# Kernel optimization log

Hardware: AMD Instinct MI355X
Metric: run time of the kernel (lower is better)

Reference implementation:

```python
import jax, jax.numpy as jnp
import numpy as np

B, S, D_MODEL = 2, 2048, 1024
N_HEADS, D_HEAD = 16, 64
ATTN_SCALE = float(np.sqrt(D_HEAD))
IGNORE = -100000.0


def setup_inputs() -> dict:
    key = jax.random.key(0)
    ks = jax.random.split(key, 8)
    scale = 1.0 / np.sqrt(D_MODEL)
    return {
        "x": jax.random.normal(ks[0], (B, S, D_MODEL), jnp.float32),
        "pos_embed": jax.random.normal(ks[1], (B, S, D_MODEL), jnp.float32),
        "W_Q": jax.random.normal(ks[2], (N_HEADS, D_MODEL, D_HEAD), jnp.float32) * scale,
        "b_Q": jnp.zeros((N_HEADS, D_HEAD), jnp.float32),
        "W_K": jax.random.normal(ks[3], (N_HEADS, D_MODEL, D_HEAD), jnp.float32) * scale,
        "b_K": jnp.zeros((N_HEADS, D_HEAD), jnp.float32),
        "W_V": jax.random.normal(ks[4], (N_HEADS, D_MODEL, D_HEAD), jnp.float32) * scale,
        "b_V": jnp.zeros((N_HEADS, D_HEAD), jnp.float32),
        "W_O": jax.random.normal(ks[5], (N_HEADS, D_HEAD, D_MODEL), jnp.float32) * (1.0 / np.sqrt(D_HEAD)),
        "b_O": jnp.zeros((D_MODEL,), jnp.float32),
    }


def reference(x, pos_embed, W_Q, b_Q, W_K, b_K, W_V, b_V, W_O, b_O):
    # use_pos_resid=False: q,k read x+pos_embed, v reads x
    attn_input = x + pos_embed                                   # [b,p,m]
    q = jnp.einsum('bpm,imh->bpih', attn_input, W_Q) + b_Q       # [b,p,i,h]
    k = jnp.einsum('bpm,imh->bpih', attn_input, W_K) + b_K
    v = jnp.einsum('bpm,imh->bpih', x, W_V) + b_V
    # scores[b,i,p,q]: query index p attends to key index q
    scores = jnp.einsum('bpih,bqih->bipq', q, k) / ATTN_SCALE
    S_len = scores.shape[-1]
    causal = jnp.tril(jnp.ones((S_len, S_len), bool))
    scores = jnp.where(causal, scores, IGNORE)
    attn = jax.nn.softmax(scores, axis=-1)                       # [b,i,q_dst,p_src]
    z = jnp.einsum('bpih,biqp->bqih', v, attn)                   # [b,q,i,h]
    out = jnp.einsum('bqih,ihm->bqm', z, W_O) + b_O              # [b,q,m]
    return out
```

## Files before the change

kernel.cpp:

```cpp
#include <hip/hip_runtime.h>
#include <hip/hip_bf16.h>
#include <stdint.h>

typedef __hip_bfloat16 bf16;
typedef __attribute__((ext_vector_type(8))) short short8;
typedef __attribute__((ext_vector_type(4))) short short4v;
typedef __attribute__((ext_vector_type(4))) float f32x4;
typedef __attribute__((ext_vector_type(16))) float f32x16;
typedef __attribute__((ext_vector_type(4))) unsigned uint4v;
typedef __attribute__((ext_vector_type(2))) unsigned uint2v;

#define AS1 __attribute__((address_space(1)))
#define AS3 __attribute__((address_space(3)))

static constexpr int SEQ = 2048, DM = 1024, DHD = 64;
static constexpr int MROWS = 2 * SEQ;

__device__ __forceinline__ short f2b(float f) {
  __hip_bfloat16 h = __float2bfloat16(f);
  return *reinterpret_cast<short*>(&h);
}

__device__ __forceinline__ unsigned pack2(float lo, float hi) {
  float2 fv; fv.x = lo; fv.y = hi;
  union { __hip_bfloat162 h; unsigned u; } cv;
  cv.h = __float22bfloat162_rn(fv);
  return cv.u;
}

__device__ __forceinline__ float fexp2(float x) {
#if __has_builtin(__builtin_amdgcn_exp2f)
  return __builtin_amdgcn_exp2f(x);
#else
  return exp2f(x);
#endif
}

union U8 { uint4v u; short8 s; };

#define GL16(dst, ptr, off) \
  asm volatile("global_load_dwordx4 %0, %1, off offset:" #off : "=v"(dst) : "v"(ptr))
#define WAITV(n) do { asm volatile("s_waitcnt vmcnt(" #n ")"); __builtin_amdgcn_sched_barrier(0); } while (0)

__device__ __forceinline__ float xmax32(float v) {
#if __has_builtin(__builtin_amdgcn_permlane32_swap)
  uint2v r = __builtin_amdgcn_permlane32_swap(__float_as_uint(v), __float_as_uint(v), false, false);
  return fmaxf(__uint_as_float(r[0]), __uint_as_float(r[1]));
#else
  return fmaxf(v, __shfl_xor(v, 32));
#endif
}
__device__ __forceinline__ float xsum32(float v) {
#if __has_builtin(__builtin_amdgcn_permlane32_swap)
  uint2v r = __builtin_amdgcn_permlane32_swap(__float_as_uint(v), __float_as_uint(v), false, false);
  return __uint_as_float(r[0]) + __uint_as_float(r[1]);
#else
  return v + __shfl_xor(v, 32);
#endif
}

__global__ __launch_bounds__(256) void prep_inputs(const float* __restrict__ x,
                                                   const float* __restrict__ pos,
                                                   bf16* __restrict__ xb,
                                                   bf16* __restrict__ aib) {
  int i = blockIdx.x * 256 + threadIdx.x;
  const int n4 = MROWS * DM / 4;
  if (i >= n4) return;
  f32x4 xv = ((const f32x4*)x)[i];
  f32x4 pv = ((const f32x4*)pos)[i];
  short4v xo, ao;
#pragma unroll
  for (int j = 0; j < 4; ++j) {
    xo[j] = f2b(xv[j]);
    ao[j] = f2b(xv[j] + pv[j]);
  }
  ((short4v*)xb)[i] = xo;
  ((short4v*)aib)[i] = ao;
}

__global__ __launch_bounds__(256) void transpose_w(const float* __restrict__ in,
                                                   bf16* __restrict__ out, int R, int C) {
  __shared__ float t[64][65];
  int ct = blockIdx.x, rt = blockIdx.y, z = blockIdx.z;
  in += (size_t)z * R * C;
  out += (size_t)z * R * C;
  int c = threadIdx.x & 63, g = threadIdx.x >> 6;
#pragma unroll
  for (int j = 0; j < 16; ++j) {
    int r = g * 16 + j;
    t[r][c] = in[(size_t)(rt * 64 + r) * C + (ct * 64 + c)];
  }
  __syncthreads();
#pragma unroll
  for (int j = 0; j < 16; ++j) {
    int rr = g * 16 + j;
    out[(size_t)(ct * 64 + rr) * R + (rt * 64 + c)] = __float2bfloat16(t[c][rr]);
  }
}

template <int MODE, typename OutT>
__device__ __forceinline__ void gemm128_body(const bf16* __restrict__ A,
                                             const bf16* __restrict__ Bt,
                                             const float* __restrict__ bias,
                                             OutT* __restrict__ C, int mt, int nt,
                                             float scale) {
  __shared__ alignas(16) bf16 Al[128 * 32];
  __shared__ alignas(16) bf16 Bl[128 * 32];
  const int lane = threadIdx.x & 63, wv = threadIdx.x >> 6;
  const int wr = wv >> 1, wc = wv & 1;
  const bf16* Ab = A + (size_t)mt * 128 * DM;
  const bf16* Bb = Bt + (size_t)nt * 128 * DM;

  f32x4 acc[4][4];
#pragma unroll
  for (int i = 0; i < 4; ++i)
#pragma unroll
    for (int j = 0; j < 4; ++j) acc[i][j] = (f32x4){0.f, 0.f, 0.f, 0.f};

  for (int kt = 0; kt < DM / 32; ++kt) {
    int k0 = kt * 32;
#pragma unroll
    for (int c = 0; c < 2; ++c) {
      int li0 = wv * 64 + c * 256;
      int li = li0 + lane;
      int row = li >> 2, sl = li & 3;
      int gs = sl ^ ((row >> 1) & 3);
      __builtin_amdgcn_global_load_lds((const AS1 void*)(Ab + (size_t)row * DM + k0 + gs * 8),
                                       (AS3 void*)(&Al[li0 * 8]), 16, 0, 0);
    }
#pragma unroll
    for (int c = 0; c < 2; ++c) {
      int li0 = wv * 64 + c * 256;
      int li = li0 + lane;
      int row = li >> 2, sl = li & 3;
      int gs = sl ^ ((row >> 1) & 3);
      __builtin_amdgcn_global_load_lds((const AS1 void*)(Bb + (size_t)row * DM + k0 + gs * 8),
                                       (AS3 void*)(&Bl[li0 * 8]), 16, 0, 0);
    }
    __syncthreads();

    short8 af[4], bfr[4];
    const int kb = lane >> 4;
#pragma unroll
    for (int mi = 0; mi < 4; ++mi) {
      int r = wr * 64 + mi * 16 + (lane & 15);
      af[mi] = *(const short8*)(&Al[r * 32 + ((kb ^ ((r >> 1) & 3)) << 3)]);
    }
#pragma unroll
    for (int ni = 0; ni < 4; ++ni) {
      int r = wc * 64 + ni * 16 + (lane & 15);
      bfr[ni] = *(const short8*)(&Bl[r * 32 + ((kb ^ ((r >> 1) & 3)) << 3)]);
    }
#pragma unroll
    for (int mi = 0; mi < 4; ++mi)
#pragma unroll
      for (int ni = 0; ni < 4; ++ni)
        acc[mi][ni] = __builtin_amdgcn_mfma_f32_16x16x32_bf16(af[mi], bfr[ni], acc[mi][ni], 0, 0, 0);
    __syncthreads();
  }

#pragma unroll
  for (int mi = 0; mi < 4; ++mi) {
#pragma unroll
    for (int ni = 0; ni < 4; ++ni) {
      int row0 = mt * 128 + wr * 64 + mi * 16 + (lane >> 4) * 4;
      int col = nt * 128 + wc * 64 + ni * 16 + (lane & 15);
      float bv = bias[col];
      if constexpr (MODE == 1) {
#pragma unroll
        for (int j = 0; j < 4; ++j)
          C[(size_t)(row0 + j) * DM + col] = (acc[mi][ni][j] + bv) * scale;
      } else {
        int bb = row0 >> 11, s0 = row0 & 2047;
        int hh = col >> 6, d0 = col & 63;
        size_t bhb = (size_t)(bb * 16 + hh) * 131072;
        if constexpr (MODE == 3) {
          int kc = d0 >> 4, hi = (d0 >> 3) & 1, e = d0 & 7;
          int g = s0 >> 5, r0 = s0 & 31;
          size_t bbase = bhb + g * 2048 + kc * 512 + e;
#pragma unroll
          for (int j = 0; j < 4; ++j)
            ((bf16*)C)[bbase + (size_t)(r0 + j + 32 * hi) * 8] =
                __float2bfloat16((acc[mi][ni][j] + bv) * scale);
        } else {
          int dj = d0 >> 5, d32 = d0 & 31;
          int ks = s0 >> 4, hi2 = (s0 >> 3) & 1, e0 = s0 & 7;
          short4v o;
#pragma unroll
          for (int j = 0; j < 4; ++j) o[j] = f2b(acc[mi][ni][j] + bv);
          *(short4v*)((bf16*)C + bhb + dj * 65536 + ks * 512 + (size_t)(d32 + 32 * hi2) * 8 + e0) = o;
        }
      }
    }
  }
}

static constexpr float QSCALE = 0.125f * 1.4426950408889634f;

__global__ __launch_bounds__(256) void qkv_gemm(const bf16* __restrict__ aib,
                                                const bf16* __restrict__ xb,
                                                const bf16* __restrict__ wqt,
                                                const bf16* __restrict__ wkt,
                                                const bf16* __restrict__ wvt,
                                                const float* __restrict__ bq,
                                                const float* __restrict__ bk,
                                                const float* __restrict__ bv,
                                                bf16* __restrict__ FQ, bf16* __restrict__ FK,
                                                bf16* __restrict__ FV) {
  int mt = blockIdx.x & 31;
  int nt = (blockIdx.x >> 5) & 7;
  int mat = blockIdx.x >> 8;
  if (mat == 0) {
    gemm128_body<3>(aib, wqt, bq, FQ, mt, nt, QSCALE);
  } else if (mat == 1) {
    gemm128_body<3>(aib, wkt, bk, FK, mt, nt, 1.0f);
  } else {
    gemm128_body<4>(xb, wvt, bv, FV, mt, nt, 1.0f);
  }
}

__global__ __launch_bounds__(256) void o_gemm64(const bf16* __restrict__ A,
                                                const bf16* __restrict__ Bt,
                                                const float* __restrict__ bias,
                                                float* __restrict__ out) {
  __shared__ alignas(16) bf16 Al[64 * 32];
  __shared__ alignas(16) bf16 Bl[128 * 32];
  const int mt = blockIdx.x & 63, nt = blockIdx.x >> 6;
  const int lane = threadIdx.x & 63, wv = threadIdx.x >> 6;
  const int wr = wv >> 1, wc = wv & 1;
  const bf16* Ab = A + (size_t)mt * 64 * DM;
  const bf16* Bb = Bt + (size_t)nt * 128 * DM;

  f32x4 acc[2][4];
#pragma unroll
  for (int i = 0; i < 2; ++i)
#pragma unroll
    for (int j = 0; j < 4; ++j) acc[i][j] = (f32x4){0.f, 0.f, 0.f, 0.f};

  for (int kt = 0; kt < DM / 32; ++kt) {
    int k0 = kt * 32;
    {
      int li0 = wv * 64;
      int li = li0 + lane;
      int row = li >> 2, sl = li & 3;
      int gs = sl ^ ((row >> 1) & 3);
      __builtin_amdgcn_global_load_lds((const AS1 void*)(Ab + (size_t)row * DM + k0 + gs * 8),
                                       (AS3 void*)(&Al[li0 * 8]), 16, 0, 0);
    }
#pragma unroll
    for (int c = 0; c < 2; ++c) {
      int li0 = wv * 64 + c * 256;
      int li = li0 + lane;
      int row = li >> 2, sl = li & 3;
      int gs = sl ^ ((row >> 1) & 3);
      __builtin_amdgcn_global_load_lds((const AS1 void*)(Bb + (size_t)row * DM + k0 + gs * 8),
                                       (AS3 void*)(&Bl[li0 * 8]), 16, 0, 0);
    }
    __syncthreads();

    short8 af[2], bfr[4];
    const int kb = lane >> 4;
#pragma unroll
    for (int mi = 0; mi < 2; ++mi) {
      int r = wr * 32 + mi * 16 + (lane & 15);
      af[mi] = *(const short8*)(&Al[r * 32 + ((kb ^ ((r >> 1) & 3)) << 3)]);
    }
#pragma unroll
    for (int ni = 0; ni < 4; ++ni) {
      int r = wc * 64 + ni * 16 + (lane & 15);
      bfr[ni] = *(const short8*)(&Bl[r * 32 + ((kb ^ ((r >> 1) & 3)) << 3)]);
    }
#pragma unroll
    for (int mi = 0; mi < 2; ++mi)
#pragma unroll
      for (int ni = 0; ni < 4; ++ni)
        acc[mi][ni] = __builtin_amdgcn_mfma_f32_16x16x32_bf16(af[mi], bfr[ni], acc[mi][ni], 0, 0, 0);
    __syncthreads();
  }

#pragma unroll
  for (int mi = 0; mi < 2; ++mi) {
#pragma unroll
    for (int ni = 0; ni < 4; ++ni) {
      int row0 = mt * 64 + wr * 32 + mi * 16 + (lane >> 4) * 4;
      int col = nt * 128 + wc * 64 + ni * 16 + (lane & 15);
      float bv = bias[col];
#pragma unroll
      for (int j = 0; j < 4; ++j)
        out[(size_t)(row0 + j) * DM + col] = acc[mi][ni][j] + bv;
    }
  }
}

__global__ __launch_bounds__(128, 2) void flash_attn(const bf16* __restrict__ FQ,
                                                     const bf16* __restrict__ FK,
                                                     const bf16* __restrict__ FV,
                                                     bf16* __restrict__ Zb) {
  __shared__ float Zm[64][33];
  __shared__ float Ml[64], Ll[64];
  __shared__ unsigned Zl[32 * 32];

  const int lane = threadIdx.x & 63;
  const int wvi = threadIdx.x >> 6;
  const int qln = lane & 31;
  const bool hib = lane >= 32;
  const int bh = blockIdx.x & 31;
  const int wq = 63 - (blockIdx.x >> 5);
  const int bb = bh >> 4, h = bh & 15;
  const int q0 = wq * 32;
  const int nt = wq / 2 + 1;
  const int hsp = (nt + 1) >> 1;
  const int t0 = wvi ? hsp : 0;
  const int t1 = wvi ? nt : hsp;

  const size_t fb = (size_t)bh * 131072;
  const bf16* qp = FQ + fb + wq * 2048 + lane * 8;
  const bf16* kpt = FK + fb + (size_t)t0 * 4096 + lane * 8;
  const bf16* vp0 = FV + fb + (size_t)t0 * 2048 + lane * 8;
  const bf16* vp1 = vp0 + 65536;

  f32x16 zacc[2];
#pragma unroll
  for (int i = 0; i < 16; ++i) { zacc[0][i] = 0.f; zacc[1][i] = 0.f; }
  float mrun = -1e30f, lrun = 0.f;

  short8 qf[4];
  short8 kfA[2][4], kfB[2][4];

  if (t0 < t1) {
    GL16(qf[0], qp, 0); GL16(qf[1], qp, 1024); GL16(qf[2], qp, 2048); GL16(qf[3], qp, 3072);
    {
      const bf16* k1 = kpt + 2048;
      GL16(kfA[0][0], kpt, 0); GL16(kfA[0][1], kpt, 1024); GL16(kfA[0][2], kpt, 2048); GL16(kfA[0][3], kpt, 3072);
      GL16(kfA[1][0], k1, 0);  GL16(kfA[1][1], k1, 1024);  GL16(kfA[1][2], k1, 2048);  GL16(kfA[1][3], k1, 3072);
      kpt += 4096;
    }

    auto computeT = [&](short8(&kf)[2][4], short8(&kfn)[2][4], int t) {
      const int kv0 = t * 64;
      const bool pref = (t + 1 < t1);

      short8 vf[2][4];
      GL16(vf[0][0], vp0, 0); GL16(vf[0][1], vp0, 1024); GL16(vf[0][2], vp0, 2048); GL16(vf[0][3], vp0, 3072);
      GL16(vf[1][0], vp1, 0); GL16(vf[1][1], vp1, 1024); GL16(vf[1][2], vp1, 2048); GL16(vf[1][3], vp1, 3072);
      vp0 += 2048; vp1 += 2048;

      WAITV(8);

      f32x16 s[2];
#pragma unroll
      for (int i = 0; i < 16; ++i) { s[0][i] = 0.f; s[1][i] = 0.f; }
#pragma unroll
      for (int kc = 0; kc < 4; ++kc) {
        s[0] = __builtin_amdgcn_mfma_f32_32x32x16_bf16(kf[0][kc], qf[kc], s[0], 0, 0, 0);
        s[1] = __builtin_amdgcn_mfma_f32_32x32x16_bf16(kf[1][kc], qf[kc], s[1], 0, 0, 0);
      }

      if (pref) {
        const bf16* k1 = kpt + 2048;
        GL16(kfn[0][0], kpt, 0); GL16(kfn[0][1], kpt, 1024); GL16(kfn[0][2], kpt, 2048); GL16(kfn[0][3], kpt, 3072);
        GL16(kfn[1][0], k1, 0);  GL16(kfn[1][1], k1, 1024);  GL16(kfn[1][2], k1, 2048);  GL16(kfn[1][3], k1, 3072);
        kpt += 4096;
      }

      if (t == nt - 1) {
        const int qg = q0 + qln;
#pragma unroll
        for (int ni = 0; ni < 2; ++ni)
#pragma unroll
          for (int rr = 0; rr < 16; ++rr) {
            int kv = kv0 + 32 * ni + (rr & 3) + 8 * (rr >> 2) + (hib ? 4 : 0);
            if (kv > qg) s[ni][rr] = -1e30f;
          }
      }

      float t8[8];
#pragma unroll
      for (int i = 0; i < 8; ++i)
        t8[i] = fmaxf(fmaxf(s[0][i], s[0][i + 8]), fmaxf(s[1][i], s[1][i + 8]));
      float tm = fmaxf(fmaxf(fmaxf(t8[0], t8[1]), fmaxf(t8[2], t8[3])),
                       fmaxf(fmaxf(t8[4], t8[5]), fmaxf(t8[6], t8[7])));
      tm = xmax32(tm);

      if (__ballot(tm > mrun + 8.0f)) {
        float mn = fmaxf(mrun, tm);
        float al = fexp2(mrun - mn);
        mrun = mn;
        lrun *= al;
#pragma unroll
        for (int i = 0; i < 16; ++i) { zacc[0][i] *= al; zacc[1][i] *= al; }
      }

      float pacc[4] = {0.f, 0.f, 0.f, 0.f};
#pragma unroll
      for (int ni = 0; ni < 2; ++ni)
#pragma unroll
        for (int rr = 0; rr < 16; ++rr) {
          float p = fexp2(s[ni][rr] - mrun);
          s[ni][rr] = p;
          pacc[rr & 3] += p;
        }
      lrun += xsum32((pacc[0] + pacc[1]) + (pacc[2] + pacc[3]));

      unsigned su32[2][8];
#pragma unroll
      for (int ni = 0; ni < 2; ++ni)
#pragma unroll
        for (int tt = 0; tt < 8; ++tt)
          su32[ni][tt] = pack2(s[ni][2 * tt], s[ni][2 * tt + 1]);

      short8 pa[4];
#if __has_builtin(__builtin_amdgcn_permlane32_swap)
#pragma unroll
      for (int c = 0; c < 4; ++c) {
        int ni = c >> 1, b4 = 4 * (c & 1);
        uint2v r0 = __builtin_amdgcn_permlane32_swap(su32[ni][b4 + 0], su32[ni][b4 + 2], false, false);
        uint2v r1 = __builtin_amdgcn_permlane32_swap(su32[ni][b4 + 1], su32[ni][b4 + 3], false, false);
        U8 w;
        w.u[0] = r0[0]; w.u[1] = r1[0]; w.u[2] = r0[1]; w.u[3] = r1[1];
        pa[c] = w.s;
      }
#else
      unsigned X[2][8];
#pragma unroll
      for (int ni = 0; ni < 2; ++ni)
#pragma unroll
        for (int tt = 0; tt < 8; ++tt)
          X[ni][tt] = (unsigned)__shfl_xor((int)su32[ni][tt], 32);
#pragma unroll
      for (int c = 0; c < 4; ++c) {
        int ni = c >> 1, b4 = 4 * (c & 1);
        U8 w;
        w.u[0] = hib ? X[ni][b4 + 2] : su32[ni][b4 + 0];
        w.u[1] = hib ? X[ni][b4 + 3] : su32[ni][b4 + 1];
        w.u[2] = hib ? su32[ni][b4 + 2] : X[ni][b4 + 0];
        w.u[3] = hib ? su32[ni][b4 + 3] : X[ni][b4 + 1];
        pa[c] = w.s;
      }
#endif

      if (pref) { WAITV(8); } else { WAITV(0); }

#pragma unroll
      for (int c = 0; c < 4; ++c) {
        zacc[0] = __builtin_amdgcn_mfma_f32_32x32x16_bf16(vf[0][c], pa[c], zacc[0], 0, 0, 0);
        zacc[1] = __builtin_amdgcn_mfma_f32_32x32x16_bf16(vf[1][c], pa[c], zacc[1], 0, 0, 0);
      }
    };

    int t = t0;
    while (true) {
      computeT(kfA, kfB, t);
      if (++t >= t1) break;
      computeT(kfB, kfA, t);
      if (++t >= t1) break;
    }
  }

  if (wvi == 1) {
#pragma unroll
    for (int i = 0; i < 16; ++i) {
      Zm[lane][i] = zacc[0][i];
      Zm[lane][16 + i] = zacc[1][i];
    }
    Ml[lane] = mrun;
    Ll[lane] = lrun;
  }
  __syncthreads();
  if (wvi == 0) {
    float m1 = Ml[lane], l1 = Ll[lane];
    float mn = fmaxf(mrun, m1);
    float a0 = fexp2(mrun - mn);
    float a1 = fexp2(m1 - mn);
    float lm = lrun * a0 + l1 * a1;
#pragma unroll
    for (int i = 0; i < 16; ++i) {
      zacc[0][i] = zacc[0][i] * a0 + Zm[lane][i] * a1;
      zacc[1][i] = zacc[1][i] * a0 + Zm[lane][16 + i] * a1;
    }

    const float rl = 1.0f / lm;
    const int W8[8] = {0, 1, 4, 5, 8, 9, 12, 13};
#pragma unroll
    for (int dj = 0; dj < 2; ++dj)
#pragma unroll
      for (int tt = 0; tt < 8; ++tt) {
        unsigned v = pack2(zacc[dj][2 * tt] * rl, zacc[dj][2 * tt + 1] * rl);
        int x = 16 * dj + (hib ? 2 : 0) + W8[tt];
        Zl[qln * 32 + (((x >> 2) ^ (qln & 7)) << 2) + (x & 3)] = v;
      }
    asm volatile("s_waitcnt lgkmcnt(0)" ::: "memory");
    __builtin_amdgcn_sched_barrier(0);
    const size_t base = ((size_t)bb * SEQ) * DM + h * DHD;
    int q2 = lane >> 1, hf = lane & 1;
#pragma unroll
    for (int u = 0; u < 4; ++u) {
      int sl = (hf * 4 + u) ^ (q2 & 7);
      U8 w;
      w.u = *(const uint4v*)&Zl[q2 * 32 + sl * 4];
      *(short8*)(Zb + base + (size_t)(q0 + q2) * DM + hf * 32 + u * 8) = w.s;
    }
  }
}

extern "C" void kernel_launch(void* const* d_in, const int* in_sizes, int n_in,
                              void* d_out, int out_size, void* d_ws, size_t ws_size,
                              hipStream_t stream) {
  (void)in_sizes; (void)n_in; (void)out_size; (void)ws_size;
  const float* x = (const float*)d_in[0];
  const float* pos = (const float*)d_in[1];
  const float* WQ = (const float*)d_in[2];
  const float* bQ = (const float*)d_in[3];
  const float* WK = (const float*)d_in[4];
  const float* bK = (const float*)d_in[5];
  const float* WV = (const float*)d_in[6];
  const float* bV = (const float*)d_in[7];
  const float* WO = (const float*)d_in[8];
  const float* bO = (const float*)d_in[9];
  float* out = (float*)d_out;

  bf16* ws = (bf16*)d_ws;
  size_t off = 0;
  bf16* aib = ws + off; off += (size_t)MROWS * DM;
  bf16* xb  = ws + off; off += (size_t)MROWS * DM;
  bf16* wqt = ws + off; off += (size_t)DM * DM;
  bf16* wkt = ws + off; off += (size_t)DM * DM;
  bf16* wvt = ws + off; off += (size_t)DM * DM;
  bf16* wot = ws + off; off += (size_t)DM * DM;
  bf16* FQ  = ws + off; off += (size_t)MROWS * DM;
  bf16* FK  = ws + off; off += (size_t)MROWS * DM;
  bf16* FV  = ws + off; off += (size_t)MROWS * DM;
  bf16* Zb  = ws + off; off += (size_t)MROWS * DM;

  prep_inputs<<<(MROWS * DM / 4 + 255) / 256, 256, 0, stream>>>(x, pos, xb, aib);
  dim3 gq(1, 16, 16);
  transpose_w<<<gq, 256, 0, stream>>>(WQ, wqt, 1024, 64);
  transpose_w<<<gq, 256, 0, stream>>>(WK, wkt, 1024, 64);
  transpose_w<<<gq, 256, 0, stream>>>(WV, wvt, 1024, 64);
  dim3 go(16, 16, 1);
  transpose_w<<<go, 256, 0, stream>>>(WO, wot, 1024, 1024);
  qkv_gemm<<<768, 256, 0, stream>>>(aib, xb, wqt, wkt, wvt, bQ, bK, bV, FQ, FK, FV);
  flash_attn<<<2048, 128, 0, stream>>>(FQ, FK, FV, Zb);
  o_gemm64<<<512, 256, 0, stream>>>(Zb, wot, bO, out);
}
```

Baseline: 113.4 us.

## Widen QKV GEMM tiles, merge weight transposes, prioritize MFMA waves in attention

The QKV projection GEMM moves from 128x128 tiles with 256 threads to 128x256 tiles with 512 threads (8 waves), so each block reuses its A tile across twice as many output columns and the grid halves to 384 blocks. The three per-head weight transposes for Q, K and V are merged into one launch with a 48-deep z dimension. The flash attention loop wraps its MFMA sections in s_setprio to raise wave priority while matrix ops issue. The trade-offs are fewer blocks for the GPU's compute units and more LDS per block.

```diff
diff --git a/kernel.cpp b/kernel.cpp
--- a/kernel.cpp
+++ b/kernel.cpp
@@ -98,18 +98,46 @@
   }
 }
 
-template <int MODE, typename OutT>
-__device__ __forceinline__ void gemm128_body(const bf16* __restrict__ A,
-                                             const bf16* __restrict__ Bt,
-                                             const float* __restrict__ bias,
-                                             OutT* __restrict__ C, int mt, int nt,
-                                             float scale) {
+__global__ __launch_bounds__(256) void transpose_w3(const float* __restrict__ wq,
+                                                    const float* __restrict__ wk,
+                                                    const float* __restrict__ wv,
+                                                    bf16* __restrict__ oq,
+                                                    bf16* __restrict__ ok,
+                                                    bf16* __restrict__ ov) {
+  __shared__ float t[64][65];
+  const int R = 1024, C = 64;
+  int rt = blockIdx.y, z = blockIdx.z;
+  const float* in = (z < 16) ? wq : (z < 32) ? wk : wv;
+  bf16* out = (z < 16) ? oq : (z < 32) ? ok : ov;
+  int zz = z & 15;
+  in += (size_t)zz * R * C;
+  out += (size_t)zz * R * C;
+  int c = threadIdx.x & 63, g = threadIdx.x >> 6;
+#pragma unroll
+  for (int j = 0; j < 16; ++j) {
+    int r = g * 16 + j;
+    t[r][c] = in[(size_t)(rt * 64 + r) * C + c];
+  }
+  __syncthreads();
+#pragma unroll
+  for (int j = 0; j < 16; ++j) {
+    int rr = g * 16 + j;
+    out[(size_t)rr * R + (rt * 64 + c)] = __float2bfloat16(t[c][rr]);
+  }
+}
+
+template <int MODE>
+__device__ __forceinline__ void qkv256_body(const bf16* __restrict__ A,
+                                            const bf16* __restrict__ Bt,
+                                            const float* __restrict__ bias,
+                                            bf16* __restrict__ C, int mt, int nt,
+                                            float scale) {
   __shared__ alignas(16) bf16 Al[128 * 32];
-  __shared__ alignas(16) bf16 Bl[128 * 32];
+  __shared__ alignas(16) bf16 Bl[256 * 32];
   const int lane = threadIdx.x & 63, wv = threadIdx.x >> 6;
-  const int wr = wv >> 1, wc = wv & 1;
+  const int wr = wv >> 2, wc = wv & 3;
   const bf16* Ab = A + (size_t)mt * 128 * DM;
-  const bf16* Bb = Bt + (size_t)nt * 128 * DM;
+  const bf16* Bb = Bt + (size_t)nt * 256 * DM;
 
   f32x4 acc[4][4];
 #pragma unroll
@@ -119,9 +147,8 @@
 
   for (int kt = 0; kt < DM / 32; ++kt) {
     int k0 = kt * 32;
-#pragma unroll
-    for (int c = 0; c < 2; ++c) {
-      int li0 = wv * 64 + c * 256;
+    {
+      int li0 = wv * 64;
       int li = li0 + lane;
       int row = li >> 2, sl = li & 3;
       int gs = sl ^ ((row >> 1) & 3);
@@ -130,7 +157,7 @@
     }
 #pragma unroll
     for (int c = 0; c < 2; ++c) {
-      int li0 = wv * 64 + c * 256;
+      int li0 = wv * 64 + c * 512;
       int li = li0 + lane;
       int row = li >> 2, sl = li & 3;
       int gs = sl ^ ((row >> 1) & 3);
@@ -164,32 +191,26 @@
 #pragma unroll
     for (int ni = 0; ni < 4; ++ni) {
       int row0 = mt * 128 + wr * 64 + mi * 16 + (lane >> 4) * 4;
-      int col = nt * 128 + wc * 64 + ni * 16 + (lane & 15);
+      int col = nt * 256 + wc * 64 + ni * 16 + (lane & 15);
       float bv = bias[col];
-      if constexpr (MODE == 1) {
+      int bb = row0 >> 11, s0 = row0 & 2047;
+      int hh = col >> 6, d0 = col & 63;
+      size_t bhb = (size_t)(bb * 16 + hh) * 131072;
+      if constexpr (MODE == 3) {
+        int kc = d0 >> 4, hi = (d0 >> 3) & 1, e = d0 & 7;
+        int g = s0 >> 5, r0 = s0 & 31;
+        size_t bbase = bhb + g * 2048 + kc * 512 + e;
 #pragma unroll
         for (int j = 0; j < 4; ++j)
-          C[(size_t)(row0 + j) * DM + col] = (acc[mi][ni][j] + bv) * scale;
+          C[bbase + (size_t)(r0 + j + 32 * hi) * 8] =
+              __float2bfloat16((acc[mi][ni][j] + bv) * scale);
       } else {
-        int bb = row0 >> 11, s0 = row0 & 2047;
-        int hh = col >> 6, d0 = col & 63;
-        size_t bhb = (size_t)(bb * 16 + hh) * 131072;
-        if constexpr (MODE == 3) {
-          int kc = d0 >> 4, hi = (d0 >> 3) & 1, e = d0 & 7;
-          int g = s0 >> 5, r0 = s0 & 31;
-          size_t bbase = bhb + g * 2048 + kc * 512 + e;
-#pragma unroll
-          for (int j = 0; j < 4; ++j)
-            ((bf16*)C)[bbase + (size_t)(r0 + j + 32 * hi) * 8] =
-                __float2bfloat16((acc[mi][ni][j] + bv) * scale);
-        } else {
-          int dj = d0 >> 5, d32 = d0 & 31;
-          int ks = s0 >> 4, hi2 = (s0 >> 3) & 1, e0 = s0 & 7;
-          short4v o;
-#pragma unroll
-          for (int j = 0; j < 4; ++j) o[j] = f2b(acc[mi][ni][j] + bv);
-          *(short4v*)((bf16*)C + bhb + dj * 65536 + ks * 512 + (size_t)(d32 + 32 * hi2) * 8 + e0) = o;
-        }
+        int dj = d0 >> 5, d32 = d0 & 31;
+        int ks = s0 >> 4, hi2 = (s0 >> 3) & 1, e0 = s0 & 7;
+        short4v o;
+#pragma unroll
+        for (int j = 0; j < 4; ++j) o[j] = f2b(acc[mi][ni][j] + bv);
+        *(short4v*)(C + bhb + dj * 65536 + ks * 512 + (size_t)(d32 + 32 * hi2) * 8 + e0) = o;
       }
     }
   }
@@ -197,7 +218,7 @@
 
 static constexpr float QSCALE = 0.125f * 1.4426950408889634f;
 
-__global__ __launch_bounds__(256) void qkv_gemm(const bf16* __restrict__ aib,
+__global__ __launch_bounds__(512) void qkv_gemm(const bf16* __restrict__ aib,
                                                 const bf16* __restrict__ xb,
                                                 const bf16* __restrict__ wqt,
                                                 const bf16* __restrict__ wkt,
@@ -208,14 +229,14 @@
                                                 bf16* __restrict__ FQ, bf16* __restrict__ FK,
                                                 bf16* __restrict__ FV) {
   int mt = blockIdx.x & 31;
-  int nt = (blockIdx.x >> 5) & 7;
-  int mat = blockIdx.x >> 8;
+  int nt = (blockIdx.x >> 5) & 3;
+  int mat = blockIdx.x >> 7;
   if (mat == 0) {
-    gemm128_body<3>(aib, wqt, bq, FQ, mt, nt, QSCALE);
+    qkv256_body<3>(aib, wqt, bq, FQ, mt, nt, QSCALE);
   } else if (mat == 1) {
-    gemm128_body<3>(aib, wkt, bk, FK, mt, nt, 1.0f);
+    qkv256_body<3>(aib, wkt, bk, FK, mt, nt, 1.0f);
   } else {
-    gemm128_body<4>(xb, wvt, bv, FV, mt, nt, 1.0f);
+    qkv256_body<4>(xb, wvt, bv, FV, mt, nt, 1.0f);
   }
 }
 
@@ -350,11 +371,13 @@
       f32x16 s[2];
 #pragma unroll
       for (int i = 0; i < 16; ++i) { s[0][i] = 0.f; s[1][i] = 0.f; }
+      __builtin_amdgcn_s_setprio(1);
 #pragma unroll
       for (int kc = 0; kc < 4; ++kc) {
         s[0] = __builtin_amdgcn_mfma_f32_32x32x16_bf16(kf[0][kc], qf[kc], s[0], 0, 0, 0);
         s[1] = __builtin_amdgcn_mfma_f32_32x32x16_bf16(kf[1][kc], qf[kc], s[1], 0, 0, 0);
       }
+      __builtin_amdgcn_s_setprio(0);
 
       if (pref) {
         const bf16* k1 = kpt + 2048;
@@ -441,11 +464,13 @@
 
       if (pref) { WAITV(8); } else { WAITV(0); }
 
+      __builtin_amdgcn_s_setprio(1);
 #pragma unroll
       for (int c = 0; c < 4; ++c) {
         zacc[0] = __builtin_amdgcn_mfma_f32_32x32x16_bf16(vf[0][c], pa[c], zacc[0], 0, 0, 0);
         zacc[1] = __builtin_amdgcn_mfma_f32_32x32x16_bf16(vf[1][c], pa[c], zacc[1], 0, 0, 0);
       }
+      __builtin_amdgcn_s_setprio(0);
     };
 
     int t = t0;
@@ -533,13 +558,11 @@
   bf16* Zb  = ws + off; off += (size_t)MROWS * DM;
 
   prep_inputs<<<(MROWS * DM / 4 + 255) / 256, 256, 0, stream>>>(x, pos, xb, aib);
-  dim3 gq(1, 16, 16);
-  transpose_w<<<gq, 256, 0, stream>>>(WQ, wqt, 1024, 64);
-  transpose_w<<<gq, 256, 0, stream>>>(WK, wkt, 1024, 64);
-  transpose_w<<<gq, 256, 0, stream>>>(WV, wvt, 1024, 64);
+  dim3 g3(1, 16, 48);
+  transpose_w3<<<g3, 256, 0, stream>>>(WQ, WK, WV, wqt, wkt, wvt);
   dim3 go(16, 16, 1);
   transpose_w<<<go, 256, 0, stream>>>(WO, wot, 1024, 1024);
-  qkv_gemm<<<768, 256, 0, stream>>>(aib, xb, wqt, wkt, wvt, bQ, bK, bV, FQ, FK, FV);
+  qkv_gemm<<<384, 512, 0, stream>>>(aib, xb, wqt, wkt, wvt, bQ, bK, bV, FQ, FK, FV);
   flash_attn<<<2048, 128, 0, stream>>>(FQ, FK, FV, Zb);
   o_gemm64<<<512, 256, 0, stream>>>(Zb, wot, bO, out);
 }
```

Result: faster. 110.7 us (-2.3%).
